# Optimization experiments

Measured on AMD Instinct MI355X. Metric: run time of the kernel, lower is better.

The kernel has to match this reference:

```python
import jax, jax.numpy as jnp
import numpy as np

B, S, DIMS, H = 1, 4096, 1024, 16
D = DIMS // H  # head dim = 64


def setup_inputs() -> dict:
    key = jax.random.key(0)
    ks = jax.random.split(key, 12)
    sc = 1.0 / np.sqrt(DIMS)
    return {
        "q": jax.random.normal(ks[0], (B, S, DIMS), jnp.float32),
        "k": jax.random.normal(ks[1], (B, S, DIMS), jnp.float32),
        "v": jax.random.normal(ks[2], (B, S, DIMS), jnp.float32),
        "mask": jax.random.randint(ks[3], (B, S, S), 0, 2, jnp.int32),
        "Wq": jax.random.normal(ks[4], (DIMS, DIMS), jnp.float32) * sc,
        "bq": jnp.zeros((DIMS,), jnp.float32),
        "Wk": jax.random.normal(ks[5], (DIMS, D), jnp.float32) * sc,
        "bk": jnp.zeros((D,), jnp.float32),
        "Wv": jax.random.normal(ks[6], (DIMS, D), jnp.float32) * sc,
        "bv": jnp.zeros((D,), jnp.float32),
        "Wo": jax.random.normal(ks[7], (DIMS, DIMS), jnp.float32) * sc,
        "bo": jnp.zeros((DIMS,), jnp.float32),
    }


def reference(q, k, v, mask, Wq, bq, Wk, bk, Wv, bv, Wo, bo):
    batch, q_len, _ = q.shape
    # projections
    qh = (q @ Wq + bq).reshape(batch, q_len, H, D)          # [B,S,H,D]
    qh = jnp.transpose(qh, (0, 2, 1, 3))                    # [B,H,S,D]
    kh = k @ Wk + bk                                        # [B,S,D] single KV head
    vh = v @ Wv + bv                                        # [B,S,D]
    # QK^T with K broadcast across heads (no explicit repeat). NOTE: original
    # module does NOT scale by 1/sqrt(D) -- keep faithful.
    scores = jnp.einsum('bhqd,bkd->bhqk', qh, kh)           # [B,H,S,S]
    scores = scores + mask[:, None, :, :].astype(scores.dtype) * jnp.asarray(-100000.0, scores.dtype)
    attn = jax.nn.softmax(scores, axis=-1)
    out = jnp.einsum('bhqk,bkd->bhqd', attn, vh)            # [B,H,S,D]
    out = jnp.transpose(out, (0, 2, 1, 3)).reshape(batch, q_len, H * D)
    out = out @ Wo + bo
    # past = first head of repeated k/v == the single-head projections
    return out, (kh, vh)
```

## Files before the change

kernel.cpp:

```cpp
#include <hip/hip_runtime.h>
#include <cstdint>
#include <cmath>

typedef _Float16 f16;
typedef _Float16 f16x4 __attribute__((ext_vector_type(4)));
typedef _Float16 f16x8 __attribute__((ext_vector_type(8)));
typedef float f32x4 __attribute__((ext_vector_type(4)));
typedef float f32x16 __attribute__((ext_vector_type(16)));
typedef uint32_t u32;
typedef uint32_t u32x4 __attribute__((ext_vector_type(4)));

#define DEVI static __device__ __forceinline__

constexpr int S  = 4096;
constexpr int DM = 1024;
constexpr int NH = 16;
constexpr int HD = 64;
constexpr float LOG2E = 1.44269504f;

DEVI void gll16(const f16* g, f16* l) {
  __builtin_amdgcn_global_load_lds((const __attribute__((address_space(1))) void*)g,
                                   (__attribute__((address_space(3))) void*)l, 16, 0, 0);
}
DEVI void wait_vm0() { asm volatile("s_waitcnt vmcnt(0)" ::: "memory"); }
DEVI u32 pkrtz(float a, float b) {
  auto h = __builtin_amdgcn_cvt_pkrtz(a, b);
  return __builtin_bit_cast(u32, h);
}
DEVI float exp2n(float x) { return __builtin_amdgcn_exp2f(x); }
#define MAX3(a,b,c) fmaxf(fmaxf(a,b),c)

__global__ void k_tcvt(const float* __restrict__ src, f16* __restrict__ dst, int R, int C) {
  __shared__ float t[32][33];
  const int c = threadIdx.x & 31, r0 = threadIdx.x >> 5;
  const int bc = blockIdx.x * 32, br = blockIdx.y * 32;
#pragma unroll
  for (int p = 0; p < 4; p++)
    t[r0 + p*8][c] = src[(size_t)(br + r0 + p*8) * C + bc + c];
  __syncthreads();
#pragma unroll
  for (int p = 0; p < 4; p++)
    dst[(size_t)(bc + r0 + p*8) * R + br + c] = (f16)t[c][r0 + p*8];
}

__global__ void k_maskbits(const int* __restrict__ m, u32* __restrict__ bits) {
  const int idx = blockIdx.x * 256 + threadIdx.x;
  const int q = idx & 4095, wc = idx >> 12;
  const int4* p = (const int4*)(m + (size_t)q * 4096 + wc * 32);
  u32 wv = 0;
#pragma unroll
  for (int j = 0; j < 8; j++) {
    int4 x = p[j];
    wv |= (x.x != 0 ? 1u : 0u) << (4*j + 0);
    wv |= (x.y != 0 ? 1u : 0u) << (4*j + 1);
    wv |= (x.z != 0 ? 1u : 0u) << (4*j + 2);
    wv |= (x.w != 0 ? 1u : 0u) << (4*j + 3);
  }
  bits[(size_t)wc * 4096 + q] = wv;
}

template<int BN, int NWM, int NWN, bool A16, int EPI>
__launch_bounds__(256)
__global__ void k_gemm(const float* __restrict__ Af, const f16* __restrict__ Ah,
                       const f16* __restrict__ Bt, const float* __restrict__ bias,
                       float* __restrict__ Cf, f16* __restrict__ Ch)
{
  constexpr int BM = 128, BK = 32, K = 1024, NW = 4;
  constexpr int WM = BM / NWM, WN = BN / NWN;
  constexpr int MM = WM / 16, NN = WN / 16;
  __shared__ __align__(16) f16 As[BM * BK];
  __shared__ __align__(16) f16 Bs[BN * BK];
  const int tid = threadIdx.x, l = tid & 63, w = tid >> 6;
  const int m0 = blockIdx.x * BM, n0 = blockIdx.y * BN;
  const int wm = (w / NWN) * WM, wn = (w % NWN) * WN;
  f32x4 acc[MM][NN] = {};

  for (int k0 = 0; k0 < K; k0 += BK) {
    if constexpr (A16) {
#pragma unroll
      for (int rep = 0; rep < 2; rep++) {
        int I = w * 2 + rep;
        gll16(Ah + (size_t)(m0 + I*16 + (l >> 2)) * K + k0 + (l & 3) * 8, &As[I * 512]);
      }
    } else {
#pragma unroll
      for (int rep = 0; rep < 2; rep++) {
        int row = (tid >> 2) + rep * 64, ko = (tid & 3) * 8;
        const float4* src = (const float4*)(Af + (size_t)(m0 + row) * K + k0 + ko);
        float4 a = src[0], b = src[1];
        f16x8 hv = { (f16)a.x,(f16)a.y,(f16)a.z,(f16)a.w,(f16)b.x,(f16)b.y,(f16)b.z,(f16)b.w };
        *(f16x8*)(&As[row * BK + ko]) = hv;
      }
    }
    constexpr int BI = (BN * BK * 2) / 1024;
#pragma unroll
    for (int rep = 0; rep < BI / NW; rep++) {
      int I = w * (BI / NW) + rep;
      gll16(Bt + (size_t)(n0 + I*16 + (l >> 2)) * K + k0 + (l & 3) * 8, &Bs[I * 512]);
    }
    wait_vm0();
    __syncthreads();
    f16x8 af[MM], bf[NN];
#pragma unroll
    for (int i = 0; i < MM; i++)
      af[i] = *(const f16x8*)(&As[(wm + i*16 + (l & 15)) * BK + (l >> 4) * 8]);
#pragma unroll
    for (int j = 0; j < NN; j++)
      bf[j] = *(const f16x8*)(&Bs[(wn + j*16 + (l & 15)) * BK + (l >> 4) * 8]);
    __builtin_amdgcn_s_setprio(1);
#pragma unroll
    for (int i = 0; i < MM; i++)
#pragma unroll
      for (int j = 0; j < NN; j++)
        acc[i][j] = __builtin_amdgcn_mfma_f32_16x16x32_f16(af[i], bf[j], acc[i][j], 0, 0, 0);
    __builtin_amdgcn_s_setprio(0);
    __syncthreads();
  }
#pragma unroll
  for (int i = 0; i < MM; i++)
#pragma unroll
    for (int j = 0; j < NN; j++)
#pragma unroll
      for (int r = 0; r < 4; r++) {
        int row = m0 + wm + i*16 + (l >> 4) * 4 + r;
        int col = n0 + wn + j*16 + (l & 15);
        float vv = acc[i][j][r] + bias[col];
        if constexpr (EPI == 0) Ch[(size_t)row * 1024 + col] = (f16)(vv * LOG2E);
        if constexpr (EPI == 1) Cf[(size_t)row * 1024 + col] = vv;
      }
}

__launch_bounds__(256)
__global__ void k_gemm_kv(const float* __restrict__ kin, const float* __restrict__ vin,
                          const f16* __restrict__ Wkt, const f16* __restrict__ Wvt,
                          const float* __restrict__ bkp, const float* __restrict__ bvp,
                          float* __restrict__ khf, float* __restrict__ vhf,
                          f16* __restrict__ khp, f16* __restrict__ vtp)
{
  constexpr int BM = 32, BK = 32, K = 1024;
  const bool isV = (blockIdx.y != 0);
  const float* A   = isV ? vin : kin;
  const f16*  Bt   = isV ? Wvt : Wkt;
  const float* bia = isV ? bvp : bkp;
  __shared__ __align__(16) f16 As[BM * BK];
  __shared__ __align__(16) f16 Bs[64 * BK];
  const int tid = threadIdx.x, l = tid & 63, w = tid >> 6;
  const int m0 = blockIdx.x * BM;
  const int wm = (w >> 1) * 16, wn = (w & 1) * 32;
  f32x4 acc[2] = {};

  for (int k0 = 0; k0 < K; k0 += BK) {
    {
      int row = tid >> 3, ko = (tid & 7) * 4;
      float4 a = *(const float4*)(A + (size_t)(m0 + row) * K + k0 + ko);
      f16x4 hv = { (f16)a.x, (f16)a.y, (f16)a.z, (f16)a.w };
      *(f16x4*)(&As[row * BK + ko]) = hv;
    }
    gll16(Bt + (size_t)(w*16 + (l >> 2)) * K + k0 + (l & 3) * 8, &Bs[w * 512]);
    wait_vm0();
    __syncthreads();
    f16x8 af = *(const f16x8*)(&As[(wm + (l & 15)) * BK + (l >> 4) * 8]);
#pragma unroll
    for (int j = 0; j < 2; j++) {
      f16x8 bf = *(const f16x8*)(&Bs[(wn + j*16 + (l & 15)) * BK + (l >> 4) * 8]);
      acc[j] = __builtin_amdgcn_mfma_f32_16x16x32_f16(af, bf, acc[j], 0, 0, 0);
    }
    __syncthreads();
  }
#pragma unroll
  for (int j = 0; j < 2; j++)
#pragma unroll
    for (int r = 0; r < 4; r++) {
      int row = m0 + wm + (l >> 4) * 4 + r;
      int col = wn + j*16 + (l & 15);
      float vv = acc[j][r] + bia[col];
      if (!isV) { khf[(size_t)row * 64 + col] = vv; khp[(size_t)row * 64 + col] = (f16)vv; }
      else      { vhf[(size_t)row * 64 + col] = vv; vtp[(size_t)col * S + row] = (f16)vv; }
    }
}

__launch_bounds__(512, 4)
__global__ void k_attn(const f16* __restrict__ qh, const f16* __restrict__ kh,
                       const f16* __restrict__ vt, const u32* __restrict__ mb,
                       f16* __restrict__ att)
{
  constexpr int KB = 64, HALF = 2048, NIT = HALF / KB;
  __shared__ __align__(16) char SM[81920];
  f16* Qs = (f16*)SM;
  f16* Ks = (f16*)(SM + 16384);
  f16* Vs = (f16*)(SM + 49152);
  float* Macc = (float*)(SM + 16384);
  float* Mml  = (float*)(SM + 49152);

  const int tid = threadIdx.x, l = tid & 63, w = tid >> 6;
  const int kvh = w >> 2, wh = w & 3;
  const int lq = l & 31, hi = l >> 5;
  const int h  = blockIdx.y * 4 + wh;
  const int q0 = blockIdx.x * 32;
  const int kvb = kvh * HALF;

  const int sch = (l & 7) ^ (l >> 3);
  const int s0  = (lq & 7) ^ (lq >> 3);
  const int s1  = s0 ^ 4;

  if (kvh == 0) {
#pragma unroll
    for (int p = 0; p < 4; p++)
      gll16(qh + (size_t)(q0 + 8*p + (l >> 3)) * DM + h * HD + (sch ^ p) * 8,
            Qs + wh * 2048 + p * 512);
  }
  f16* KsH = Ks + kvh * 8192;
  f16* VsH = Vs + kvh * 8192;
#pragma unroll
  for (int j = 0; j < 2; j++) {
    const int row = 16*wh + 8*j + (l >> 3);
    const int sc = sch ^ (2*wh + j);
    gll16(kh + (size_t)(kvb + row) * HD + sc * 8, KsH + (2*wh + j) * 512);
    gll16(vt + (size_t)row * S + kvb + sc * 8,    VsH + (2*wh + j) * 512);
  }
  wait_vm0();
  __syncthreads();

  f32x16 acc0 = {}, acc1 = {};
  float mrun = -1e29f, lsum = 0.f;
  const f16* QsW = Qs + wh * 2048;

  for (int it = 0; it < NIT; ++it) {
    const int cur = it & 1;
    const int wd = (kvb >> 5) + it * 2;
    u32 mw0 = mb[(size_t)wd * S + q0 + lq];
    u32 mw1 = mb[(size_t)(wd + 1) * S + q0 + lq];
    if (it + 1 < NIT) {
      const int nk = kvb + (it + 1) * KB;
#pragma unroll
      for (int j = 0; j < 2; j++) {
        const int row = 16*wh + 8*j + (l >> 3);
        const int sc = sch ^ (2*wh + j);
        gll16(kh + (size_t)(nk + row) * HD + sc * 8, KsH + (cur ^ 1) * 4096 + (2*wh + j) * 512);
        gll16(vt + (size_t)row * S + nk + sc * 8,    VsH + (cur ^ 1) * 4096 + (2*wh + j) * 512);
      }
    }
    f32x16 t0 = {}, t1 = {};
    const f16* KT = KsH + cur * 4096;
    __builtin_amdgcn_s_setprio(1);
#pragma unroll
    for (int c = 0; c < 4; c++) {
      const int u = hi + 2 * c;
      f16x8 qfc = *(const f16x8*)(QsW + lq * 64 + ((u ^ s0) << 3));
      f16x8 kf0 = *(const f16x8*)(KT + lq * 64        + ((u ^ s0) << 3));
      f16x8 kf1 = *(const f16x8*)(KT + (32 + lq) * 64 + ((u ^ s1) << 3));
      t0 = __builtin_amdgcn_mfma_f32_32x32x16_f16(kf0, qfc, t0, 0, 0, 0);
      t1 = __builtin_amdgcn_mfma_f32_32x32x16_f16(kf1, qfc, t1, 0, 0, 0);
    }
    __builtin_amdgcn_s_setprio(0);
    const u32 b0 = mw0 >> (4 * hi), b1 = mw1 >> (4 * hi);
#pragma unroll
    for (int r = 0; r < 16; r++) {
      const int bp = (r & 3) + 8 * (r >> 2);
      t0[r] = ((b0 >> bp) & 1) ? -1e30f : t0[r];
      t1[r] = ((b1 >> bp) & 1) ? -1e30f : t1[r];
    }
    float z0 = MAX3(t0[0], t0[1],  t0[2]),  z1 = MAX3(t0[3],  t0[4],  t0[5]);
    float z2 = MAX3(t0[6], t0[7],  t0[8]),  z3 = MAX3(t0[9],  t0[10], t0[11]);
    float z4 = MAX3(t0[12],t0[13], t0[14]), z5 = MAX3(t0[15], t1[0],  t1[1]);
    float z6 = MAX3(t1[2], t1[3],  t1[4]),  z7 = MAX3(t1[5],  t1[6],  t1[7]);
    float z8 = MAX3(t1[8], t1[9],  t1[10]), z9 = MAX3(t1[11], t1[12], t1[13]);
    float za = fmaxf(t1[14], t1[15]);
    float y0 = MAX3(z0, z1, z2), y1 = MAX3(z3, z4, z5), y2 = MAX3(z6, z7, z8);
    float pmax = MAX3(y0, y1, fmaxf(y2, fmaxf(z9, za)));
    pmax = fmaxf(pmax, __shfl_xor(pmax, 32));
    if (!__all(pmax <= mrun + 11.6f)) {
      float mn = fmaxf(mrun, pmax);
      float sc = exp2n(mrun - mn);
      mrun = mn; lsum *= sc;
#pragma unroll
      for (int r = 0; r < 16; r++) { acc0[r] *= sc; acc1[r] *= sc; }
    }
#pragma unroll
    for (int r = 0; r < 16; r++) {
      t0[r] = exp2n(t0[r] - mrun);
      t1[r] = exp2n(t1[r] - mrun);
    }
    {
      float a0s = 0.f, a1s = 0.f, a2s = 0.f, a3s = 0.f;
#pragma unroll
      for (int r = 0; r < 16; r += 4) {
        a0s += t0[r] + t1[r];       a1s += t0[r+1] + t1[r+1];
        a2s += t0[r+2] + t1[r+2];   a3s += t0[r+3] + t1[r+3];
      }
      float rs = (a0s + a1s) + (a2s + a3s);
      rs += __shfl_xor(rs, 32);
      lsum += rs;
    }
    const f16* VT = VsH + cur * 4096;
#pragma unroll
    for (int c = 0; c < 4; c++) {
      const int cc = c & 1;
      u32 w0, w1, w2, w3;
      if (c < 2) {
        w0 = pkrtz(t0[8*cc + 0], t0[8*cc + 1]);  w2 = pkrtz(t0[8*cc + 4], t0[8*cc + 5]);
        w1 = pkrtz(t0[8*cc + 2], t0[8*cc + 3]);  w3 = pkrtz(t0[8*cc + 6], t0[8*cc + 7]);
      } else {
        w0 = pkrtz(t1[8*cc + 0], t1[8*cc + 1]);  w2 = pkrtz(t1[8*cc + 4], t1[8*cc + 5]);
        w1 = pkrtz(t1[8*cc + 2], t1[8*cc + 3]);  w3 = pkrtz(t1[8*cc + 6], t1[8*cc + 7]);
      }
      asm volatile("v_permlane32_swap_b32 %0, %1" : "+v"(w0), "+v"(w2));
      asm volatile("v_permlane32_swap_b32 %0, %1" : "+v"(w1), "+v"(w3));
      u32x4 aw = { w0, w1, w2, w3 };
      f16x8 pa = __builtin_bit_cast(f16x8, aw);
      const int u = hi + 2 * c;
      f16x8 v0 = *(const f16x8*)(VT + lq * 64        + ((u ^ s0) << 3));
      f16x8 v1 = *(const f16x8*)(VT + (32 + lq) * 64 + ((u ^ s1) << 3));
      __builtin_amdgcn_s_setprio(1);
      acc0 = __builtin_amdgcn_mfma_f32_32x32x16_f16(v0, pa, acc0, 0, 0, 0);
      acc1 = __builtin_amdgcn_mfma_f32_32x32x16_f16(v1, pa, acc1, 0, 0, 0);
      __builtin_amdgcn_s_setprio(0);
    }
    wait_vm0();
    __syncthreads();
  }

  if (kvh == 1) {
#pragma unroll
    for (int r = 0; r < 16; r++) {
      const int d0 = (r & 3) + 8 * (r >> 2) + 4 * hi;
      Macc[wh * 2048 + d0 * 32 + lq]        = acc0[r];
      Macc[wh * 2048 + (d0 + 32) * 32 + lq] = acc1[r];
    }
    if (hi == 0) {
      Mml[wh * 64 + lq]      = mrun;
      Mml[wh * 64 + 32 + lq] = lsum;
    }
  }
  __syncthreads();
  if (kvh == 0) {
    const float mB = Mml[wh * 64 + lq];
    const float lB = Mml[wh * 64 + 32 + lq];
    const float mS = fmaxf(mrun, mB);
    const float eA = exp2n(mrun - mS), eB = exp2n(mB - mS);
    const float inv = 1.f / (lsum * eA + lB * eB);
    const float fA = eA * inv, fB = eB * inv;
    const size_t base = (size_t)(q0 + lq) * DM + h * HD;
#pragma unroll
    for (int g = 0; g < 4; g++) {
      f16x4 o0, o1;
#pragma unroll
      for (int j = 0; j < 4; j++) {
        const int r = 4 * g + j, d0 = j + 8 * g + 4 * hi;
        o0[j] = (f16)(acc0[r] * fA + Macc[wh * 2048 + d0 * 32 + lq] * fB);
        o1[j] = (f16)(acc1[r] * fA + Macc[wh * 2048 + (d0 + 32) * 32 + lq] * fB);
      }
      *(f16x4*)(att + base + 8 * g + 4 * hi)      = o0;
      *(f16x4*)(att + base + 32 + 8 * g + 4 * hi) = o1;
    }
  }
}

extern "C" void kernel_launch(void* const* d_in, const int* in_sizes, int n_in,
                              void* d_out, int out_size, void* d_ws, size_t ws_size,
                              hipStream_t stream)
{
  const float* q  = (const float*)d_in[0];
  const float* k  = (const float*)d_in[1];
  const float* v  = (const float*)d_in[2];
  const int*  msk = (const int*)d_in[3];
  const float* Wq = (const float*)d_in[4];
  const float* bq = (const float*)d_in[5];
  const float* Wk = (const float*)d_in[6];
  const float* bk = (const float*)d_in[7];
  const float* Wv = (const float*)d_in[8];
  const float* bv = (const float*)d_in[9];
  const float* Wo = (const float*)d_in[10];
  const float* bo = (const float*)d_in[11];

  float* out = (float*)d_out;
  float* khf = out + (size_t)S * DM;
  float* vhf = khf + (size_t)S * HD;

  char* ws = (char*)d_ws;
  f16* Wq_t = (f16*)(ws);
  f16* Wo_t = (f16*)(ws + (2u  << 20));
  f16* Wk_t = (f16*)(ws + (4u  << 20));
  f16* Wv_t = (f16*)(ws + (4u  << 20) + (128u << 10));
  f16* qhp  = (f16*)(ws + (4u  << 20) + (256u << 10));
  f16* khp  = (f16*)(ws + (12u << 20) + (256u << 10));
  f16* vtp  = (f16*)(ws + (12u << 20) + (768u << 10));
  f16* attp = (f16*)(ws + (13u << 20) + (256u << 10));
  u32* mbp  = (u32*)(ws + (21u << 20) + (256u << 10));

  k_tcvt<<<dim3(32, 32), 256, 0, stream>>>(Wq, Wq_t, 1024, 1024);
  k_tcvt<<<dim3(32, 32), 256, 0, stream>>>(Wo, Wo_t, 1024, 1024);
  k_tcvt<<<dim3(2, 32),  256, 0, stream>>>(Wk, Wk_t, 1024, 64);
  k_tcvt<<<dim3(2, 32),  256, 0, stream>>>(Wv, Wv_t, 1024, 64);
  k_maskbits<<<2048, 256, 0, stream>>>(msk, mbp);

  k_gemm<128, 2, 2, false, 0><<<dim3(32, 8), 256, 0, stream>>>(q, nullptr, Wq_t, bq, nullptr, qhp);
  k_gemm_kv<<<dim3(128, 2), 256, 0, stream>>>(k, v, Wk_t, Wv_t, bk, bv, khf, vhf, khp, vtp);

  k_attn<<<dim3(S / 32, 4), 512, 0, stream>>>(qhp, khp, vtp, mbp, attp);

  k_gemm<128, 2, 2, true, 1><<<dim3(32, 8), 256, 0, stream>>>(nullptr, attp, Wo_t, bo, out, nullptr);
}
```

Before: 208.9 us.

## Replace KV-split attention with 64-query blocks sharing one full KV stream

The attention kernel no longer splits the key range into two halves merged through shared memory. Each block now handles 64 queries (two 32-query groups) across 4 heads and streams the whole K/V sequence once, with all 8 waves cooperatively loading each K/V tile. Q fragments are kept in registers instead of LDS, which cuts LDS use to 32 KB and drops the final cross-half merge. In exchange the grid halves to 256 blocks and each block runs twice as many iterations, which can leave the GPU underfilled and lengthen the serial loop.

Result: slower. 230.4 us (+10.3%).

```diff
diff --git a/kernel.cpp b/kernel.cpp
--- a/kernel.cpp
+++ b/kernel.cpp
@@ -1,6 +1,5 @@
 #include <hip/hip_runtime.h>
 #include <cstdint>
-#include <cmath>
 
 typedef _Float16 f16;
 typedef _Float16 f16x4 __attribute__((ext_vector_type(4)));
@@ -184,73 +183,54 @@
                        const f16* __restrict__ vt, const u32* __restrict__ mb,
                        f16* __restrict__ att)
 {
-  constexpr int KB = 64, HALF = 2048, NIT = HALF / KB;
-  __shared__ __align__(16) char SM[81920];
-  f16* Qs = (f16*)SM;
-  f16* Ks = (f16*)(SM + 16384);
-  f16* Vs = (f16*)(SM + 49152);
-  float* Macc = (float*)(SM + 16384);
-  float* Mml  = (float*)(SM + 49152);
+  constexpr int KB = 64, NIT = S / KB;
+  __shared__ __align__(16) f16 Ks[2][64 * 64];
+  __shared__ __align__(16) f16 Vs[2][64 * 64];
 
   const int tid = threadIdx.x, l = tid & 63, w = tid >> 6;
-  const int kvh = w >> 2, wh = w & 3;
+  const int qt = w >> 2, wh = w & 3;
   const int lq = l & 31, hi = l >> 5;
   const int h  = blockIdx.y * 4 + wh;
-  const int q0 = blockIdx.x * 32;
-  const int kvb = kvh * HALF;
-
-  const int sch = (l & 7) ^ (l >> 3);
+  const int q0 = blockIdx.x * 64 + qt * 32;
+
+  const int sch = (l & 7) ^ (l >> 3) ^ w;
   const int s0  = (lq & 7) ^ (lq >> 3);
   const int s1  = s0 ^ 4;
-
-  if (kvh == 0) {
-#pragma unroll
-    for (int p = 0; p < 4; p++)
-      gll16(qh + (size_t)(q0 + 8*p + (l >> 3)) * DM + h * HD + (sch ^ p) * 8,
-            Qs + wh * 2048 + p * 512);
-  }
-  f16* KsH = Ks + kvh * 8192;
-  f16* VsH = Vs + kvh * 8192;
-#pragma unroll
-  for (int j = 0; j < 2; j++) {
-    const int row = 16*wh + 8*j + (l >> 3);
-    const int sc = sch ^ (2*wh + j);
-    gll16(kh + (size_t)(kvb + row) * HD + sc * 8, KsH + (2*wh + j) * 512);
-    gll16(vt + (size_t)row * S + kvb + sc * 8,    VsH + (2*wh + j) * 512);
-  }
+  const int srow = 8 * w + (l >> 3);
+
+  f16x8 qf[4];
+#pragma unroll
+  for (int c = 0; c < 4; c++)
+    qf[c] = *(const f16x8*)(qh + (size_t)(q0 + lq) * DM + h * HD + c * 16 + hi * 8);
+
+  gll16(kh + (size_t)srow * HD + sch * 8, &Ks[0][w * 512]);
+  gll16(vt + (size_t)srow * S  + sch * 8, &Vs[0][w * 512]);
   wait_vm0();
   __syncthreads();
 
   f32x16 acc0 = {}, acc1 = {};
   float mrun = -1e29f, lsum = 0.f;
-  const f16* QsW = Qs + wh * 2048;
 
   for (int it = 0; it < NIT; ++it) {
     const int cur = it & 1;
-    const int wd = (kvb >> 5) + it * 2;
+    const int wd = it * 2;
     u32 mw0 = mb[(size_t)wd * S + q0 + lq];
     u32 mw1 = mb[(size_t)(wd + 1) * S + q0 + lq];
     if (it + 1 < NIT) {
-      const int nk = kvb + (it + 1) * KB;
-#pragma unroll
-      for (int j = 0; j < 2; j++) {
-        const int row = 16*wh + 8*j + (l >> 3);
-        const int sc = sch ^ (2*wh + j);
-        gll16(kh + (size_t)(nk + row) * HD + sc * 8, KsH + (cur ^ 1) * 4096 + (2*wh + j) * 512);
-        gll16(vt + (size_t)row * S + nk + sc * 8,    VsH + (cur ^ 1) * 4096 + (2*wh + j) * 512);
-      }
+      const int nk = (it + 1) * KB;
+      gll16(kh + (size_t)(nk + srow) * HD + sch * 8, &Ks[cur ^ 1][w * 512]);
+      gll16(vt + (size_t)srow * S + nk + sch * 8,    &Vs[cur ^ 1][w * 512]);
     }
     f32x16 t0 = {}, t1 = {};
-    const f16* KT = KsH + cur * 4096;
+    const f16* KT = &Ks[cur][0];
     __builtin_amdgcn_s_setprio(1);
 #pragma unroll
     for (int c = 0; c < 4; c++) {
       const int u = hi + 2 * c;
-      f16x8 qfc = *(const f16x8*)(QsW + lq * 64 + ((u ^ s0) << 3));
       f16x8 kf0 = *(const f16x8*)(KT + lq * 64        + ((u ^ s0) << 3));
       f16x8 kf1 = *(const f16x8*)(KT + (32 + lq) * 64 + ((u ^ s1) << 3));
-      t0 = __builtin_amdgcn_mfma_f32_32x32x16_f16(kf0, qfc, t0, 0, 0, 0);
-      t1 = __builtin_amdgcn_mfma_f32_32x32x16_f16(kf1, qfc, t1, 0, 0, 0);
+      t0 = __builtin_amdgcn_mfma_f32_32x32x16_f16(kf0, qf[c], t0, 0, 0, 0);
+      t1 = __builtin_amdgcn_mfma_f32_32x32x16_f16(kf1, qf[c], t1, 0, 0, 0);
     }
     __builtin_amdgcn_s_setprio(0);
     const u32 b0 = mw0 >> (4 * hi), b1 = mw1 >> (4 * hi);
@@ -292,7 +272,7 @@
       rs += __shfl_xor(rs, 32);
       lsum += rs;
     }
-    const f16* VT = VsH + cur * 4096;
+    const f16* VT = &Vs[cur][0];
 #pragma unroll
     for (int c = 0; c < 4; c++) {
       const int cc = c & 1;
@@ -320,39 +300,19 @@
     __syncthreads();
   }
 
-  if (kvh == 1) {
-#pragma unroll
-    for (int r = 0; r < 16; r++) {
-      const int d0 = (r & 3) + 8 * (r >> 2) + 4 * hi;
-      Macc[wh * 2048 + d0 * 32 + lq]        = acc0[r];
-      Macc[wh * 2048 + (d0 + 32) * 32 + lq] = acc1[r];
-    }
-    if (hi == 0) {
-      Mml[wh * 64 + lq]      = mrun;
-      Mml[wh * 64 + 32 + lq] = lsum;
-    }
-  }
-  __syncthreads();
-  if (kvh == 0) {
-    const float mB = Mml[wh * 64 + lq];
-    const float lB = Mml[wh * 64 + 32 + lq];
-    const float mS = fmaxf(mrun, mB);
-    const float eA = exp2n(mrun - mS), eB = exp2n(mB - mS);
-    const float inv = 1.f / (lsum * eA + lB * eB);
-    const float fA = eA * inv, fB = eB * inv;
-    const size_t base = (size_t)(q0 + lq) * DM + h * HD;
-#pragma unroll
-    for (int g = 0; g < 4; g++) {
-      f16x4 o0, o1;
-#pragma unroll
-      for (int j = 0; j < 4; j++) {
-        const int r = 4 * g + j, d0 = j + 8 * g + 4 * hi;
-        o0[j] = (f16)(acc0[r] * fA + Macc[wh * 2048 + d0 * 32 + lq] * fB);
-        o1[j] = (f16)(acc1[r] * fA + Macc[wh * 2048 + (d0 + 32) * 32 + lq] * fB);
-      }
-      *(f16x4*)(att + base + 8 * g + 4 * hi)      = o0;
-      *(f16x4*)(att + base + 32 + 8 * g + 4 * hi) = o1;
-    }
+  const float inv = 1.f / lsum;
+  const size_t base = (size_t)(q0 + lq) * DM + h * HD;
+#pragma unroll
+  for (int g = 0; g < 4; g++) {
+    f16x4 o0, o1;
+#pragma unroll
+    for (int j = 0; j < 4; j++) {
+      const int r = 4 * g + j;
+      o0[j] = (f16)(acc0[r] * inv);
+      o1[j] = (f16)(acc1[r] * inv);
+    }
+    *(f16x4*)(att + base + 8 * g + 4 * hi)      = o0;
+    *(f16x4*)(att + base + 32 + 8 * g + 4 * hi) = o1;
   }
 }
 
@@ -397,7 +357,7 @@
   k_gemm<128, 2, 2, false, 0><<<dim3(32, 8), 256, 0, stream>>>(q, nullptr, Wq_t, bq, nullptr, qhp);
   k_gemm_kv<<<dim3(128, 2), 256, 0, stream>>>(k, v, Wk_t, Wv_t, bk, bv, khf, vhf, khp, vtp);
 
-  k_attn<<<dim3(S / 32, 4), 512, 0, stream>>>(qhp, khp, vtp, mbp, attp);
+  k_attn<<<dim3(S / 64, 4), 512, 0, stream>>>(qhp, khp, vtp, mbp, attp);
 
   k_gemm<128, 2, 2, true, 1><<<dim3(32, 8), 256, 0, stream>>>(nullptr, attp, Wo_t, bo, out, nullptr);
 }
```
